# Kernel optimization log

Measured on AMD Instinct MI355X. Metric: run time of the kernel, lower is better.

## Reference

```python
import jax, jax.numpy as jnp
import numpy as np

H, W = 16, 16  # input_resolution
NUM_HEADS = 16
DIM = 512


def build_relative_position_index(h, w):
    coords = np.stack(np.meshgrid(np.arange(h), np.arange(w), indexing='ij'))  # [2,h,w]
    cf = coords.reshape(2, -1)
    rel = cf[:, :, None] - cf[:, None, :]            # [2,N,N]
    rel = rel.transpose(1, 2, 0).astype(np.int32)    # [N,N,2]
    rel[:, :, 0] += h - 1
    rel[:, :, 1] += w - 1
    rel[:, :, 0] *= 2 * w - 1
    return jnp.asarray(rel.sum(-1).reshape(-1), dtype=jnp.int32)  # [N*N]


def setup_inputs() -> dict:
    key = jax.random.key(0)
    ks = jax.random.split(key, 6)
    B, N, C = 128, H * W, DIM
    x = jax.random.normal(ks[0], (B, N, C), dtype=jnp.float32)
    qkv_w = jax.random.normal(ks[1], (3 * C, C), dtype=jnp.float32) * (C ** -0.5)
    qkv_b = jax.random.normal(ks[2], (3 * C,), dtype=jnp.float32) * 0.02
    proj_w = jax.random.normal(ks[3], (C, C), dtype=jnp.float32) * (C ** -0.5)
    proj_b = jax.random.normal(ks[4], (C,), dtype=jnp.float32) * 0.02
    bias_table = jax.random.normal(ks[5], ((2 * H - 1) * (2 * W - 1), NUM_HEADS), dtype=jnp.float32) * 0.02
    rel_index = build_relative_position_index(H, W)
    return {"x": x, "qkv_w": qkv_w, "qkv_b": qkv_b, "proj_w": proj_w,
            "proj_b": proj_b, "bias_table": bias_table, "rel_index": rel_index}


def reference(x, qkv_w, qkv_b, proj_w, proj_b, bias_table, rel_index):
    B, N, C = x.shape
    h = NUM_HEADS
    hd = C // h
    scale = hd ** -0.5
    # qkv projection: [B,N,3C] -> [3,B,h,N,hd]
    qkv = (jnp.einsum('bnc,oc->bno', x, qkv_w) + qkv_b)
    qkv = qkv.reshape(B, N, 3, h, hd).transpose(2, 0, 3, 1, 4)
    q, k, v = qkv[0], qkv[1], qkv[2]
    # relative position bias: gather [N*N,h] -> [1,h,N,N]
    bias = bias_table[rel_index].reshape(N, N, h).transpose(2, 0, 1)[None]
    attn = jnp.einsum('bhnd,bhmd->bhnm', q * scale, k) + bias
    attn = jax.nn.softmax(attn, axis=-1)
    out = jnp.einsum('bhnm,bhmd->bhnd', attn, v)     # [B,h,N,hd]
    out = out.transpose(0, 2, 1, 3).reshape(B, N, C)
    return jnp.einsum('bnc,oc->bno', out, proj_w) + proj_b
```

## Files before the change

### kernel.cpp

```cpp
#include <hip/hip_runtime.h>

typedef __bf16 bf16_t;
typedef __bf16 bf16x8 __attribute__((ext_vector_type(8)));
typedef float f32x4 __attribute__((ext_vector_type(4)));

#define MFMA_16x16x32(a, b, c) __builtin_amdgcn_mfma_f32_16x16x32_bf16((a), (b), (c), 0, 0, 0)

__device__ inline bf16x8 cvt8(const float* __restrict__ p) {
  bf16x8 r;
#pragma unroll
  for (int j = 0; j < 8; j++) r[j] = (bf16_t)p[j];
  return r;
}

__device__ inline void load_lds16(const bf16_t* g, bf16_t* l) {
  __builtin_amdgcn_global_load_lds(
      (const __attribute__((address_space(1))) void*)g,
      (__attribute__((address_space(3))) void*)l, 16, 0, 0);
}

__global__ __launch_bounds__(256) void convert_k(
    const float* __restrict__ x, const float* __restrict__ qkv_w,
    const float* __restrict__ proj_w,
    bf16_t* __restrict__ xbf, bf16_t* __restrict__ wqkvbf,
    bf16_t* __restrict__ wprojbf) {
  size_t base = ((size_t)blockIdx.x * 256 + threadIdx.x) * 8;
  if (base < 16777216) {
    *(bf16x8*)(xbf + base) = cvt8(x + base);
  } else if (base < 17563648) {
    size_t o = base - 16777216;
    *(bf16x8*)(wqkvbf + o) = cvt8(qkv_w + o);
  } else {
    size_t o = base - 17563648;
    *(bf16x8*)(wprojbf + o) = cvt8(proj_w + o);
  }
}

__global__ __launch_bounds__(256) void bias_gather_k(
    const float* __restrict__ table, const int* __restrict__ rel,
    float* __restrict__ biasws) {
  int idx = blockIdx.x * 256 + threadIdx.x;
  int h = idx >> 16;
  int rem = idx & 65535;
  int qb = rem >> 12;
  int ct = (rem >> 8) & 15;
  int L = (rem >> 2) & 63;
  int r = idx & 3;
  int q = qb * 16 + (L & 15);
  int k = ct * 16 + (L >> 4) * 4 + r;
  biasws[idx] = table[rel[q * 256 + k] * 16 + h];
}

#define PH_OPEN() __builtin_amdgcn_s_setprio(1)

#define PH_CLOSE()                                        \
  do {                                                    \
    __builtin_amdgcn_s_setprio(0);                        \
    asm volatile("s_waitcnt lgkmcnt(0)" ::: "memory");    \
    __builtin_amdgcn_sched_barrier(0);                    \
    __builtin_amdgcn_s_barrier();                         \
    __builtin_amdgcn_sched_barrier(0);                    \
  } while (0)

#define GATE4()                                           \
  do {                                                    \
    __builtin_amdgcn_s_setprio(0);                        \
    asm volatile("s_waitcnt vmcnt(4)" ::: "memory");      \
    __builtin_amdgcn_s_barrier();                         \
    __builtin_amdgcn_sched_barrier(0);                    \
  } while (0)

#define GATE0()                                           \
  do {                                                    \
    __builtin_amdgcn_s_setprio(0);                        \
    asm volatile("s_waitcnt vmcnt(0)" ::: "memory");      \
    __builtin_amdgcn_s_barrier();                         \
    __builtin_amdgcn_sched_barrier(0);                    \
  } while (0)

#define STG2(src, dst, c)                                                        \
  do {                                                                           \
    load_lds16((src) + (c)*32768, (dst) + (c)*4096);                             \
    load_lds16((src) + ((c) + 1) * 32768, (dst) + ((c) + 1) * 4096);             \
  } while (0)

#define RDA(dst, buf, ibase)                                                     \
  _Pragma("unroll") for (int i = 0; i < 4; ++i) {                                \
    dst[i][0] = *(const bf16x8*)&As[(buf)*16384 + a0 + ((ibase) + i) * 1024];    \
    dst[i][1] = *(const bf16x8*)&As[(buf)*16384 + a1 + ((ibase) + i) * 1024];    \
  }
#define RDB(dst, buf, jbase)                                                     \
  _Pragma("unroll") for (int j = 0; j < 2; ++j) {                                \
    dst[j][0] = *(const bf16x8*)&Bs[(buf)*16384 + b0 + ((jbase) + j) * 1024];    \
    dst[j][1] = *(const bf16x8*)&Bs[(buf)*16384 + b1 + ((jbase) + j) * 1024];    \
  }

#define MFQ(Af, Bf, I0, J0)                                                      \
  _Pragma("unroll") for (int i = 0; i < 4; ++i) _Pragma("unroll")                \
      for (int j = 0; j < 2; ++j) {                                              \
    acc[(I0) + i][(J0) + j] =                                                    \
        MFMA_16x16x32(Af[i][0], Bf[j][0], acc[(I0) + i][(J0) + j]);              \
    acc[(I0) + i][(J0) + j] =                                                    \
        MFMA_16x16x32(Af[i][1], Bf[j][1], acc[(I0) + i][(J0) + j]);              \
  }

#define GEMM_SETUP(Ap, Wp)                                                       \
  __shared__ bf16_t As[2 * 16384];                                               \
  __shared__ bf16_t Bs[2 * 16384];                                               \
  const int t = threadIdx.x;                                                     \
  const int w = t >> 6, L = t & 63;                                              \
  const int wm = w >> 2, wn = w & 3;                                             \
  const int lrow = L & 15, lq = L >> 4;                                          \
  const int srow = t >> 3;                                                       \
  const int sslot = (t & 7) ^ (srow & 7);                                        \
  const bf16_t* ga = (Ap) + (size_t)(m0 + srow) * 512 + sslot * 8;               \
  const bf16_t* gb = (Wp) + (size_t)(n0 + srow) * 512 + sslot * 8;               \
  bf16_t* la = As + t * 8;                                                       \
  bf16_t* lb = Bs + t * 8;                                                       \
  const int m8 = (lrow & 7) * 8;                                                 \
  const int a0 = (wm * 128 + lrow) * 64 + ((lq * 8) ^ m8);                       \
  const int a1 = (wm * 128 + lrow) * 64 + ((32 + lq * 8) ^ m8);                  \
  const int b0 = (wn * 64 + lrow) * 64 + ((lq * 8) ^ m8);                        \
  const int b1 = (wn * 64 + lrow) * 64 + ((32 + lq * 8) ^ m8);

#define PROLOGUE()                                                               \
  STG2(ga, la, 0); STG2(ga, la, 2);                                              \
  STG2(gb, lb, 0); STG2(gb, lb, 2);                                              \
  STG2(ga + 64, la + 16384, 0); STG2(ga + 64, la + 16384, 2);                    \
  asm volatile("s_waitcnt vmcnt(4)" ::: "memory");                               \
  __builtin_amdgcn_s_barrier();                                                  \
  __builtin_amdgcn_sched_barrier(0);

#define HALF_STEADY(CUR, LBDST, LADST, GBP, GAP)                                 \
  {                                                                              \
    bf16x8 fal[4][2], fbl[2][2], fah[4][2], fbh[2][2];                           \
    RDA(fal, CUR, 0); RDB(fbl, CUR, 0); RDB(fbh, CUR, 2);                        \
    STG2(GBP, LBDST, 0);                                                         \
    PH_OPEN(); MFQ(fal, fbl, 0, 0); PH_CLOSE();                                  \
    RDA(fah, CUR, 4);                                                            \
    STG2(GBP, LBDST, 2);                                                         \
    PH_OPEN(); MFQ(fal, fbh, 0, 2); PH_CLOSE();                                  \
    STG2(GAP, LADST, 0);                                                         \
    PH_OPEN(); MFQ(fah, fbh, 4, 2); PH_CLOSE();                                  \
    STG2(GAP, LADST, 2);                                                         \
    PH_OPEN(); MFQ(fah, fbl, 4, 0); GATE4();                                     \
  }

#define GEMM_LOOP()                                                              \
  {                                                                              \
    const bf16_t* gA = ga + 128;                                       \
    const bf16_t* gB = gb + 64;                                        \
    _Pragma("unroll 1") for (int G = 0; G < 3; ++G) {                            \
      HALF_STEADY(0, lb + 16384, la, gB, gA)                                     \
      HALF_STEADY(1, lb, la + 16384, gB + 64, gA + 64)                           \
      gA += 128; gB += 128;                                                      \
    }                                                                            \
    {            \
      bf16x8 fal[4][2], fbl[2][2], fah[4][2], fbh[2][2];                         \
      RDA(fal, 0, 0); RDB(fbl, 0, 0); RDB(fbh, 0, 2);                            \
      STG2(gB, lb + 16384, 0);                                                   \
      PH_OPEN(); MFQ(fal, fbl, 0, 0); PH_CLOSE();                                \
      RDA(fah, 0, 4);                                                            \
      STG2(gB, lb + 16384, 2);                                                   \
      PH_OPEN(); MFQ(fal, fbh, 0, 2); PH_CLOSE();                                \
      PH_OPEN(); MFQ(fah, fbh, 4, 2); PH_CLOSE();                                \
      PH_OPEN(); MFQ(fah, fbl, 4, 0); GATE0();                                   \
    }                                                                            \
    {                               \
      bf16x8 fal[4][2], fbl[2][2], fah[4][2], fbh[2][2];                         \
      RDA(fal, 1, 0); RDB(fbl, 1, 0); RDB(fbh, 1, 2);                            \
      PH_OPEN(); MFQ(fal, fbl, 0, 0); PH_CLOSE();                                \
      RDA(fah, 1, 4);                                                            \
      PH_OPEN(); MFQ(fal, fbh, 0, 2); PH_CLOSE();                                \
      PH_OPEN(); MFQ(fah, fbh, 4, 2); PH_CLOSE();                                \
      PH_OPEN(); MFQ(fah, fbl, 4, 0);                                            \
      __builtin_amdgcn_s_setprio(0);                                             \
      __builtin_amdgcn_sched_barrier(0);                                         \
    }                                                                            \
  }

__global__ __launch_bounds__(512, 2) void qkv_gemm256_k(
    const bf16_t* __restrict__ A, const bf16_t* __restrict__ W,
    const float* __restrict__ Bvec,
    bf16_t* __restrict__ qws, bf16_t* __restrict__ kws, bf16_t* __restrict__ vws) {
  const int id = blockIdx.x;
  const int wg = (id & 7) * 96 + (id >> 3);
  const int mt = wg / 6, nt = wg % 6;
  const int m0 = mt * 256, n0 = nt * 256;

  GEMM_SETUP(A, W);

  f32x4 acc[8][4];
#pragma unroll
  for (int jj = 0; jj < 4; ++jj) {
    float bv = Bvec[n0 + wn * 64 + jj * 16 + lrow];
#pragma unroll
    for (int i = 0; i < 8; ++i) acc[i][jj] = (f32x4){bv, bv, bv, bv};
  }

  PROLOGUE();
  GEMM_LOOP();

  const int col0 = n0 + wn * 64;
  const int s = col0 >> 9;
  bf16_t* dst = (s == 0) ? qws : (s == 1) ? kws : vws;
  const float mul = (s == 0) ? 0.17677669529663687f : 1.0f;
#pragma unroll
  for (int jj = 0; jj < 4; ++jj) {
    int o = col0 + jj * 16 + lrow;
    int rem = o & 511;
    int hh = rem >> 5, d = rem & 31;
#pragma unroll
    for (int i = 0; i < 8; ++i) {
#pragma unroll
      for (int r = 0; r < 4; ++r) {
        int m = m0 + wm * 128 + i * 16 + lq * 4 + r;
        int b = m >> 8, n = m & 255;
        dst[(size_t)(((b * 16 + hh) * 256 + n) << 5) + d] =
            (bf16_t)(acc[i][jj][r] * mul);
      }
    }
  }
}

__global__ __launch_bounds__(512, 2) void proj_gemm256_k(
    const bf16_t* __restrict__ A, const bf16_t* __restrict__ W,
    const float* __restrict__ Bvec, float* __restrict__ out) {
  const int id = blockIdx.x;
  const int lin = (id & 7) * 32 + (id >> 3);
  const int mt = lin >> 1, nt = lin & 1;
  const int m0 = mt * 256, n0 = nt * 256;

  GEMM_SETUP(A, W);

  f32x4 acc[8][4];
#pragma unroll
  for (int jj = 0; jj < 4; ++jj) {
    float bv = Bvec[n0 + wn * 64 + jj * 16 + lrow];
#pragma unroll
    for (int i = 0; i < 8; ++i) acc[i][jj] = (f32x4){bv, bv, bv, bv};
  }

  PROLOGUE();
  GEMM_LOOP();

#pragma unroll
  for (int jj = 0; jj < 4; ++jj) {
    int o = n0 + wn * 64 + jj * 16 + lrow;
#pragma unroll
    for (int i = 0; i < 8; ++i) {
#pragma unroll
      for (int r = 0; r < 4; ++r) {
        int m = m0 + wm * 128 + i * 16 + lq * 4 + r;
        out[(size_t)m * 512 + o] = acc[i][jj][r];
      }
    }
  }
}

__global__ __launch_bounds__(256) void attn_k(
    const bf16_t* __restrict__ qws, const bf16_t* __restrict__ kws,
    const bf16_t* __restrict__ vws, const float* __restrict__ biasws,
    bf16_t* __restrict__ aows) {
  __shared__ __align__(16) bf16_t Vs[32 * 264];

  const int bh = blockIdx.x;
  const int h = bh & 15, b = bh >> 4;

  const int t = threadIdx.x;
  const int w = t >> 6, L = t & 63;
  const int lrow = L & 15, lq = L >> 4;

  const bf16_t* kbase = kws + (size_t)bh * 8192;
  const bf16_t* vbase = vws + (size_t)bh * 8192;

#pragma unroll
  for (int c = 0; c < 4; c++) {
    bf16x8 vv = *(const bf16x8*)(vbase + t * 32 + c * 8);
#pragma unroll
    for (int j = 0; j < 8; j++) Vs[(c * 8 + j) * 264 + t] = vv[j];
  }
  __syncthreads();

  const int idxA = ((2 * (lq & 1)) * 16 + lrow) * 4;
  const int idxB = idxA + 64;
  const bool gsel = (lq < 2);

  const float* bbw = biasws + h * 65536 + (w * 4) * 4096;

#pragma unroll 1
  for (int s = 0; s < 4; ++s) {
    const int qrow0 = w * 64 + s * 16;
    const bf16_t* qbase = qws + (size_t)bh * 8192 + qrow0 * 32;
    bf16x8 qf = *(const bf16x8*)(qbase + lrow * 32 + lq * 8);
    const float* bb = bbw + s * 4096;

    f32x4 S[16];
#pragma unroll
    for (int ct = 0; ct < 16; ct++) {
      bf16x8 kf = *(const bf16x8*)(kbase + (ct * 16 + lrow) * 32 + lq * 8);
      f32x4 bi = *(const f32x4*)(bb + ct * 256 + L * 4);
      S[ct] = MFMA_16x16x32(kf, qf, bi);
    }

    float sm = 0.f;
#pragma unroll
    for (int ct = 0; ct < 16; ct++)
#pragma unroll
      for (int r = 0; r < 4; r++) {
        float e = __expf(S[ct][r]);
        S[ct][r] = e;
        sm += e;
      }
    sm += __shfl_xor(sm, 16, 64);
    sm += __shfl_xor(sm, 32, 64);
    const float inv = 1.0f / sm;

    int pd[16][2];
#pragma unroll
    for (int ct = 0; ct < 16; ct++) {
#pragma unroll
      for (int j = 0; j < 2; j++) {
        float lo = S[ct][2 * j] * inv;
        float hi = S[ct][2 * j + 1] * inv;
        int d;
        asm("v_cvt_pk_bf16_f32 %0, %1, %2" : "=v"(d) : "v"(lo), "v"(hi));
        pd[ct][j] = d;
      }
    }

    f32x4 O0 = {}, O1 = {};
#pragma unroll
    for (int kt = 0; kt < 8; kt++) {
      int rA0 = __builtin_amdgcn_ds_bpermute(idxA, pd[2 * kt][0]);
      int rA1 = __builtin_amdgcn_ds_bpermute(idxA, pd[2 * kt][1]);
      int rA2 = __builtin_amdgcn_ds_bpermute(idxB, pd[2 * kt][0]);
      int rA3 = __builtin_amdgcn_ds_bpermute(idxB, pd[2 * kt][1]);
      int rB0 = __builtin_amdgcn_ds_bpermute(idxA, pd[2 * kt + 1][0]);
      int rB1 = __builtin_amdgcn_ds_bpermute(idxA, pd[2 * kt + 1][1]);
      int rB2 = __builtin_amdgcn_ds_bpermute(idxB, pd[2 * kt + 1][0]);
      int rB3 = __builtin_amdgcn_ds_bpermute(idxB, pd[2 * kt + 1][1]);
      int4 Di;
      Di.x = gsel ? rA0 : rB0;
      Di.y = gsel ? rA1 : rB1;
      Di.z = gsel ? rA2 : rB2;
      Di.w = gsel ? rA3 : rB3;
      bf16x8 pf = *reinterpret_cast<bf16x8*>(&Di);
      bf16x8 v0 = *(const bf16x8*)&Vs[lrow * 264 + kt * 32 + lq * 8];
      bf16x8 v1 = *(const bf16x8*)&Vs[(16 + lrow) * 264 + kt * 32 + lq * 8];
      O0 = MFMA_16x16x32(pf, v0, O0);
      O1 = MFMA_16x16x32(pf, v1, O1);
    }

    bf16_t* obase = aows + (size_t)(b * 256 + qrow0) * 512 + h * 32;
#pragma unroll
    for (int r = 0; r < 4; r++) {
      int rl = lq * 4 + r;
      obase[rl * 512 + lrow] = (bf16_t)(O0[r]);
      obase[rl * 512 + 16 + lrow] = (bf16_t)(O1[r]);
    }
  }
}

extern "C" void kernel_launch(void* const* d_in, const int* in_sizes, int n_in,
                              void* d_out, int out_size, void* d_ws, size_t ws_size,
                              hipStream_t stream) {
  (void)in_sizes; (void)n_in; (void)out_size; (void)ws_size;
  const float* x      = (const float*)d_in[0];
  const float* qkv_w  = (const float*)d_in[1];
  const float* qkv_b  = (const float*)d_in[2];
  const float* proj_w = (const float*)d_in[3];
  const float* proj_b = (const float*)d_in[4];
  const float* table  = (const float*)d_in[5];
  const int*   rel    = (const int*)d_in[6];

  const size_t QKV_ELEMS = 16777216;
  bf16_t* qws     = (bf16_t*)d_ws;
  bf16_t* kws     = qws + QKV_ELEMS;
  bf16_t* vws     = kws + QKV_ELEMS;
  float*  biasws  = (float*)(vws + QKV_ELEMS);
  bf16_t* wqkvbf  = (bf16_t*)(biasws + 1048576);
  bf16_t* wprojbf = wqkvbf + 786432;
  bf16_t* xbf     = wprojbf + 262144;
  bf16_t* aows    = xbf;
  float*  out     = (float*)d_out;

  convert_k<<<8704, 256, 0, stream>>>(x, qkv_w, proj_w, xbf, wqkvbf, wprojbf);
  bias_gather_k<<<4096, 256, 0, stream>>>(table, rel, biasws);
  qkv_gemm256_k<<<768, 512, 0, stream>>>(xbf, wqkvbf, qkv_b, qws, kws, vws);
  attn_k<<<2048, 256, 0, stream>>>(qws, kws, vws, biasws, aows);
  proj_gemm256_k<<<256, 512, 0, stream>>>(aows, wprojbf, proj_b, out);
}
```

Measured before the change: 295.8 us.

## Shrink GEMM tiles to 128x128, fuse prep kernels, use exp2 softmax with deferred normalization

Both GEMMs move from 256x256 tiles with 512 threads to 128x128 tiles with 256 threads, giving more blocks for better CU fill and shorter tails at the cost of less data reuse per tile. The conversion and bias-gather kernels are merged into one launch to save a launch. Softmax now uses raw v_exp_f32 (base 2), with log2e folded into the q scale and the bias table. Normalization moves from every probability to the final output rows via a bpermute of the inverse sum, and the row sum uses vector partial sums.

```diff
diff --git a/kernel.cpp b/kernel.cpp
--- a/kernel.cpp
+++ b/kernel.cpp
@@ -5,6 +5,7 @@
 typedef float f32x4 __attribute__((ext_vector_type(4)));
 
 #define MFMA_16x16x32(a, b, c) __builtin_amdgcn_mfma_f32_16x16x32_bf16((a), (b), (c), 0, 0, 0)
+#define LOG2E 1.4426950408889634f
 
 __device__ inline bf16x8 cvt8(const float* __restrict__ p) {
   bf16x8 r;
@@ -19,36 +20,36 @@
       (__attribute__((address_space(3))) void*)l, 16, 0, 0);
 }
 
-__global__ __launch_bounds__(256) void convert_k(
+__global__ __launch_bounds__(256) void prep_k(
     const float* __restrict__ x, const float* __restrict__ qkv_w,
-    const float* __restrict__ proj_w,
+    const float* __restrict__ proj_w, const float* __restrict__ table,
+    const int* __restrict__ rel,
     bf16_t* __restrict__ xbf, bf16_t* __restrict__ wqkvbf,
-    bf16_t* __restrict__ wprojbf) {
-  size_t base = ((size_t)blockIdx.x * 256 + threadIdx.x) * 8;
-  if (base < 16777216) {
-    *(bf16x8*)(xbf + base) = cvt8(x + base);
-  } else if (base < 17563648) {
-    size_t o = base - 16777216;
-    *(bf16x8*)(wqkvbf + o) = cvt8(qkv_w + o);
+    bf16_t* __restrict__ wprojbf, float* __restrict__ biasws) {
+  const int bid = blockIdx.x;
+  if (bid < 8704) {
+    size_t base = ((size_t)bid * 256 + threadIdx.x) * 8;
+    if (base < 16777216) {
+      *(bf16x8*)(xbf + base) = cvt8(x + base);
+    } else if (base < 17563648) {
+      size_t o = base - 16777216;
+      *(bf16x8*)(wqkvbf + o) = cvt8(qkv_w + o);
+    } else {
+      size_t o = base - 17563648;
+      *(bf16x8*)(wprojbf + o) = cvt8(proj_w + o);
+    }
   } else {
-    size_t o = base - 17563648;
-    *(bf16x8*)(wprojbf + o) = cvt8(proj_w + o);
-  }
-}
-
-__global__ __launch_bounds__(256) void bias_gather_k(
-    const float* __restrict__ table, const int* __restrict__ rel,
-    float* __restrict__ biasws) {
-  int idx = blockIdx.x * 256 + threadIdx.x;
-  int h = idx >> 16;
-  int rem = idx & 65535;
-  int qb = rem >> 12;
-  int ct = (rem >> 8) & 15;
-  int L = (rem >> 2) & 63;
-  int r = idx & 3;
-  int q = qb * 16 + (L & 15);
-  int k = ct * 16 + (L >> 4) * 4 + r;
-  biasws[idx] = table[rel[q * 256 + k] * 16 + h];
+    int idx = (bid - 8704) * 256 + threadIdx.x;
+    int h = idx >> 16;
+    int rem = idx & 65535;
+    int qb = rem >> 12;
+    int ct = (rem >> 8) & 15;
+    int L = (rem >> 2) & 63;
+    int r = idx & 3;
+    int q = qb * 16 + (L & 15);
+    int k = ct * 16 + (L >> 4) * 4 + r;
+    biasws[idx] = table[rel[q * 256 + k] * 16 + h] * LOG2E;
+  }
 }
 
 #define PH_OPEN() __builtin_amdgcn_s_setprio(1)
@@ -80,23 +81,23 @@
 
 #define STG2(src, dst, c)                                                        \
   do {                                                                           \
-    load_lds16((src) + (c)*32768, (dst) + (c)*4096);                             \
-    load_lds16((src) + ((c) + 1) * 32768, (dst) + ((c) + 1) * 4096);             \
+    load_lds16((src) + (c)*16384, (dst) + (c)*2048);                             \
+    load_lds16((src) + ((c) + 1) * 16384, (dst) + ((c) + 1) * 2048);             \
   } while (0)
 
-#define RDA(dst, buf, ibase)                                                     \
-  _Pragma("unroll") for (int i = 0; i < 4; ++i) {                                \
-    dst[i][0] = *(const bf16x8*)&As[(buf)*16384 + a0 + ((ibase) + i) * 1024];    \
-    dst[i][1] = *(const bf16x8*)&As[(buf)*16384 + a1 + ((ibase) + i) * 1024];    \
-  }
-#define RDB(dst, buf, jbase)                                                     \
+#define RDA2(dst, buf, ibase)                                                    \
+  _Pragma("unroll") for (int i = 0; i < 2; ++i) {                                \
+    dst[i][0] = *(const bf16x8*)&As[(buf)*8192 + a0 + ((ibase) + i) * 1024];     \
+    dst[i][1] = *(const bf16x8*)&As[(buf)*8192 + a1 + ((ibase) + i) * 1024];     \
+  }
+#define RDB2(dst, buf, jbase)                                                    \
   _Pragma("unroll") for (int j = 0; j < 2; ++j) {                                \
-    dst[j][0] = *(const bf16x8*)&Bs[(buf)*16384 + b0 + ((jbase) + j) * 1024];    \
-    dst[j][1] = *(const bf16x8*)&Bs[(buf)*16384 + b1 + ((jbase) + j) * 1024];    \
-  }
-
-#define MFQ(Af, Bf, I0, J0)                                                      \
-  _Pragma("unroll") for (int i = 0; i < 4; ++i) _Pragma("unroll")                \
+    dst[j][0] = *(const bf16x8*)&Bs[(buf)*8192 + b0 + ((jbase) + j) * 1024];     \
+    dst[j][1] = *(const bf16x8*)&Bs[(buf)*8192 + b1 + ((jbase) + j) * 1024];     \
+  }
+
+#define MFQ2(Af, Bf, I0, J0)                                                     \
+  _Pragma("unroll") for (int i = 0; i < 2; ++i) _Pragma("unroll")                \
       for (int j = 0; j < 2; ++j) {                                              \
     acc[(I0) + i][(J0) + j] =                                                    \
         MFMA_16x16x32(Af[i][0], Bf[j][0], acc[(I0) + i][(J0) + j]);              \
@@ -105,11 +106,11 @@
   }
 
 #define GEMM_SETUP(Ap, Wp)                                                       \
-  __shared__ bf16_t As[2 * 16384];                                               \
-  __shared__ bf16_t Bs[2 * 16384];                                               \
+  __shared__ bf16_t As[2 * 8192];                                                \
+  __shared__ bf16_t Bs[2 * 8192];                                                \
   const int t = threadIdx.x;                                                     \
   const int w = t >> 6, L = t & 63;                                              \
-  const int wm = w >> 2, wn = w & 3;                                             \
+  const int wm = w >> 1, wn = w & 1;                                             \
   const int lrow = L & 15, lq = L >> 4;                                          \
   const int srow = t >> 3;                                                       \
   const int sslot = (t & 7) ^ (srow & 7);                                        \
@@ -118,32 +119,32 @@
   bf16_t* la = As + t * 8;                                                       \
   bf16_t* lb = Bs + t * 8;                                                       \
   const int m8 = (lrow & 7) * 8;                                                 \
-  const int a0 = (wm * 128 + lrow) * 64 + ((lq * 8) ^ m8);                       \
-  const int a1 = (wm * 128 + lrow) * 64 + ((32 + lq * 8) ^ m8);                  \
+  const int a0 = (wm * 64 + lrow) * 64 + ((lq * 8) ^ m8);                        \
+  const int a1 = (wm * 64 + lrow) * 64 + ((32 + lq * 8) ^ m8);                   \
   const int b0 = (wn * 64 + lrow) * 64 + ((lq * 8) ^ m8);                        \
   const int b1 = (wn * 64 + lrow) * 64 + ((32 + lq * 8) ^ m8);
 
 #define PROLOGUE()                                                               \
   STG2(ga, la, 0); STG2(ga, la, 2);                                              \
   STG2(gb, lb, 0); STG2(gb, lb, 2);                                              \
-  STG2(ga + 64, la + 16384, 0); STG2(ga + 64, la + 16384, 2);                    \
+  STG2(ga + 64, la + 8192, 0); STG2(ga + 64, la + 8192, 2);                      \
   asm volatile("s_waitcnt vmcnt(4)" ::: "memory");                               \
   __builtin_amdgcn_s_barrier();                                                  \
   __builtin_amdgcn_sched_barrier(0);
 
 #define HALF_STEADY(CUR, LBDST, LADST, GBP, GAP)                                 \
   {                                                                              \
-    bf16x8 fal[4][2], fbl[2][2], fah[4][2], fbh[2][2];                           \
-    RDA(fal, CUR, 0); RDB(fbl, CUR, 0); RDB(fbh, CUR, 2);                        \
+    bf16x8 fal[2][2], fbl[2][2], fah[2][2], fbh[2][2];                           \
+    RDA2(fal, CUR, 0); RDB2(fbl, CUR, 0); RDB2(fbh, CUR, 2);                     \
     STG2(GBP, LBDST, 0);                                                         \
-    PH_OPEN(); MFQ(fal, fbl, 0, 0); PH_CLOSE();                                  \
-    RDA(fah, CUR, 4);                                                            \
+    PH_OPEN(); MFQ2(fal, fbl, 0, 0); PH_CLOSE();                                 \
+    RDA2(fah, CUR, 2);                                                           \
     STG2(GBP, LBDST, 2);                                                         \
-    PH_OPEN(); MFQ(fal, fbh, 0, 2); PH_CLOSE();                                  \
+    PH_OPEN(); MFQ2(fal, fbh, 0, 2); PH_CLOSE();                                 \
     STG2(GAP, LADST, 0);                                                         \
-    PH_OPEN(); MFQ(fah, fbh, 4, 2); PH_CLOSE();                                  \
+    PH_OPEN(); MFQ2(fah, fbh, 2, 2); PH_CLOSE();                                 \
     STG2(GAP, LADST, 2);                                                         \
-    PH_OPEN(); MFQ(fah, fbl, 4, 0); GATE4();                                     \
+    PH_OPEN(); MFQ2(fah, fbl, 2, 0); GATE4();                                    \
   }
 
 #define GEMM_LOOP()                                                              \
@@ -151,51 +152,51 @@
     const bf16_t* gA = ga + 128;                                       \
     const bf16_t* gB = gb + 64;                                        \
     _Pragma("unroll 1") for (int G = 0; G < 3; ++G) {                            \
-      HALF_STEADY(0, lb + 16384, la, gB, gA)                                     \
-      HALF_STEADY(1, lb, la + 16384, gB + 64, gA + 64)                           \
+      HALF_STEADY(0, lb + 8192, la, gB, gA)                                      \
+      HALF_STEADY(1, lb, la + 8192, gB + 64, gA + 64)                            \
       gA += 128; gB += 128;                                                      \
     }                                                                            \
     {            \
-      bf16x8 fal[4][2], fbl[2][2], fah[4][2], fbh[2][2];                         \
-      RDA(fal, 0, 0); RDB(fbl, 0, 0); RDB(fbh, 0, 2);                            \
-      STG2(gB, lb + 16384, 0);                                                   \
-      PH_OPEN(); MFQ(fal, fbl, 0, 0); PH_CLOSE();                                \
-      RDA(fah, 0, 4);                                                            \
-      STG2(gB, lb + 16384, 2);                                                   \
-      PH_OPEN(); MFQ(fal, fbh, 0, 2); PH_CLOSE();                                \
-      PH_OPEN(); MFQ(fah, fbh, 4, 2); PH_CLOSE();                                \
-      PH_OPEN(); MFQ(fah, fbl, 4, 0); GATE0();                                   \
+      bf16x8 fal[2][2], fbl[2][2], fah[2][2], fbh[2][2];                         \
+      RDA2(fal, 0, 0); RDB2(fbl, 0, 0); RDB2(fbh, 0, 2);                         \
+      STG2(gB, lb + 8192, 0);                                                    \
+      PH_OPEN(); MFQ2(fal, fbl, 0, 0); PH_CLOSE();                               \
+      RDA2(fah, 0, 2);                                                           \
+      STG2(gB, lb + 8192, 2);                                                    \
+      PH_OPEN(); MFQ2(fal, fbh, 0, 2); PH_CLOSE();                               \
+      PH_OPEN(); MFQ2(fah, fbh, 2, 2); PH_CLOSE();                               \
+      PH_OPEN(); MFQ2(fah, fbl, 2, 0); GATE0();                                  \
     }                                                                            \
     {                               \
-      bf16x8 fal[4][2], fbl[2][2], fah[4][2], fbh[2][2];                         \
-      RDA(fal, 1, 0); RDB(fbl, 1, 0); RDB(fbh, 1, 2);                            \
-      PH_OPEN(); MFQ(fal, fbl, 0, 0); PH_CLOSE();                                \
-      RDA(fah, 1, 4);                                                            \
-      PH_OPEN(); MFQ(fal, fbh, 0, 2); PH_CLOSE();                                \
-      PH_OPEN(); MFQ(fah, fbh, 4, 2); PH_CLOSE();                                \
-      PH_OPEN(); MFQ(fah, fbl, 4, 0);                                            \
+      bf16x8 fal[2][2], fbl[2][2], fah[2][2], fbh[2][2];                         \
+      RDA2(fal, 1, 0); RDB2(fbl, 1, 0); RDB2(fbh, 1, 2);                         \
+      PH_OPEN(); MFQ2(fal, fbl, 0, 0); PH_CLOSE();                               \
+      RDA2(fah, 1, 2);                                                           \
+      PH_OPEN(); MFQ2(fal, fbh, 0, 2); PH_CLOSE();                               \
+      PH_OPEN(); MFQ2(fah, fbh, 2, 2); PH_CLOSE();                               \
+      PH_OPEN(); MFQ2(fah, fbl, 2, 0);                                           \
       __builtin_amdgcn_s_setprio(0);                                             \
       __builtin_amdgcn_sched_barrier(0);                                         \
     }                                                                            \
   }
 
-__global__ __launch_bounds__(512, 2) void qkv_gemm256_k(
+__global__ __launch_bounds__(256, 2) void qkv_gemm128_k(
     const bf16_t* __restrict__ A, const bf16_t* __restrict__ W,
     const float* __restrict__ Bvec,
     bf16_t* __restrict__ qws, bf16_t* __restrict__ kws, bf16_t* __restrict__ vws) {
   const int id = blockIdx.x;
-  const int wg = (id & 7) * 96 + (id >> 3);
-  const int mt = wg / 6, nt = wg % 6;
-  const int m0 = mt * 256, n0 = nt * 256;
+  const int wg = (id & 7) * 384 + (id >> 3);
+  const int mt = wg / 12, nt = wg % 12;
+  const int m0 = mt * 128, n0 = nt * 128;
 
   GEMM_SETUP(A, W);
 
-  f32x4 acc[8][4];
+  f32x4 acc[4][4];
 #pragma unroll
   for (int jj = 0; jj < 4; ++jj) {
     float bv = Bvec[n0 + wn * 64 + jj * 16 + lrow];
 #pragma unroll
-    for (int i = 0; i < 8; ++i) acc[i][jj] = (f32x4){bv, bv, bv, bv};
+    for (int i = 0; i < 4; ++i) acc[i][jj] = (f32x4){bv, bv, bv, bv};
   }
 
   PROLOGUE();
@@ -204,17 +205,17 @@
   const int col0 = n0 + wn * 64;
   const int s = col0 >> 9;
   bf16_t* dst = (s == 0) ? qws : (s == 1) ? kws : vws;
-  const float mul = (s == 0) ? 0.17677669529663687f : 1.0f;
+  const float mul = (s == 0) ? 0.17677669529663687f * LOG2E : 1.0f;
 #pragma unroll
   for (int jj = 0; jj < 4; ++jj) {
     int o = col0 + jj * 16 + lrow;
     int rem = o & 511;
     int hh = rem >> 5, d = rem & 31;
 #pragma unroll
-    for (int i = 0; i < 8; ++i) {
+    for (int i = 0; i < 4; ++i) {
 #pragma unroll
       for (int r = 0; r < 4; ++r) {
-        int m = m0 + wm * 128 + i * 16 + lq * 4 + r;
+        int m = m0 + wm * 64 + i * 16 + lq * 4 + r;
         int b = m >> 8, n = m & 255;
         dst[(size_t)(((b * 16 + hh) * 256 + n) << 5) + d] =
             (bf16_t)(acc[i][jj][r] * mul);
@@ -223,22 +224,22 @@
   }
 }
 
-__global__ __launch_bounds__(512, 2) void proj_gemm256_k(
+__global__ __launch_bounds__(256, 2) void proj_gemm128_k(
     const bf16_t* __restrict__ A, const bf16_t* __restrict__ W,
     const float* __restrict__ Bvec, float* __restrict__ out) {
   const int id = blockIdx.x;
-  const int lin = (id & 7) * 32 + (id >> 3);
-  const int mt = lin >> 1, nt = lin & 1;
-  const int m0 = mt * 256, n0 = nt * 256;
+  const int wg = (id & 7) * 128 + (id >> 3);
+  const int mt = wg >> 2, nt = wg & 3;
+  const int m0 = mt * 128, n0 = nt * 128;
 
   GEMM_SETUP(A, W);
 
-  f32x4 acc[8][4];
+  f32x4 acc[4][4];
 #pragma unroll
   for (int jj = 0; jj < 4; ++jj) {
     float bv = Bvec[n0 + wn * 64 + jj * 16 + lrow];
 #pragma unroll
-    for (int i = 0; i < 8; ++i) acc[i][jj] = (f32x4){bv, bv, bv, bv};
+    for (int i = 0; i < 4; ++i) acc[i][jj] = (f32x4){bv, bv, bv, bv};
   }
 
   PROLOGUE();
@@ -248,10 +249,10 @@
   for (int jj = 0; jj < 4; ++jj) {
     int o = n0 + wn * 64 + jj * 16 + lrow;
 #pragma unroll
-    for (int i = 0; i < 8; ++i) {
+    for (int i = 0; i < 4; ++i) {
 #pragma unroll
       for (int r = 0; r < 4; ++r) {
-        int m = m0 + wm * 128 + i * 16 + lq * 4 + r;
+        int m = m0 + wm * 64 + i * 16 + lq * 4 + r;
         out[(size_t)m * 512 + o] = acc[i][jj][r];
       }
     }
@@ -303,15 +304,18 @@
       S[ct] = MFMA_16x16x32(kf, qf, bi);
     }
 
-    float sm = 0.f;
-#pragma unroll
-    for (int ct = 0; ct < 16; ct++)
+    f32x4 sv = {};
+#pragma unroll
+    for (int ct = 0; ct < 16; ct++) {
 #pragma unroll
       for (int r = 0; r < 4; r++) {
-        float e = __expf(S[ct][r]);
+        float e;
+        asm("v_exp_f32 %0, %1" : "=v"(e) : "v"(S[ct][r]));
         S[ct][r] = e;
-        sm += e;
       }
+      sv += S[ct];
+    }
+    float sm = (sv[0] + sv[1]) + (sv[2] + sv[3]);
     sm += __shfl_xor(sm, 16, 64);
     sm += __shfl_xor(sm, 32, 64);
     const float inv = 1.0f / sm;
@@ -321,10 +325,9 @@
     for (int ct = 0; ct < 16; ct++) {
 #pragma unroll
       for (int j = 0; j < 2; j++) {
-        float lo = S[ct][2 * j] * inv;
-        float hi = S[ct][2 * j + 1] * inv;
         int d;
-        asm("v_cvt_pk_bf16_f32 %0, %1, %2" : "=v"(d) : "v"(lo), "v"(hi));
+        asm("v_cvt_pk_bf16_f32 %0, %1, %2"
+            : "=v"(d) : "v"(S[ct][2 * j]), "v"(S[ct][2 * j + 1]));
         pd[ct][j] = d;
       }
     }
@@ -355,9 +358,11 @@
     bf16_t* obase = aows + (size_t)(b * 256 + qrow0) * 512 + h * 32;
 #pragma unroll
     for (int r = 0; r < 4; r++) {
+      float invO = __int_as_float(
+          __builtin_amdgcn_ds_bpermute((lq * 4 + r) * 4, __float_as_int(inv)));
       int rl = lq * 4 + r;
-      obase[rl * 512 + lrow] = (bf16_t)(O0[r]);
-      obase[rl * 512 + 16 + lrow] = (bf16_t)(O1[r]);
+      obase[rl * 512 + lrow] = (bf16_t)(O0[r] * invO);
+      obase[rl * 512 + 16 + lrow] = (bf16_t)(O1[r] * invO);
     }
   }
 }
@@ -385,9 +390,9 @@
   bf16_t* aows    = xbf;
   float*  out     = (float*)d_out;
 
-  convert_k<<<8704, 256, 0, stream>>>(x, qkv_w, proj_w, xbf, wqkvbf, wprojbf);
-  bias_gather_k<<<4096, 256, 0, stream>>>(table, rel, biasws);
-  qkv_gemm256_k<<<768, 512, 0, stream>>>(xbf, wqkvbf, qkv_b, qws, kws, vws);
+  prep_k<<<12800, 256, 0, stream>>>(x, qkv_w, proj_w, table, rel,
+                                    xbf, wqkvbf, wprojbf, biasws);
+  qkv_gemm128_k<<<3072, 256, 0, stream>>>(xbf, wqkvbf, qkv_b, qws, kws, vws);
   attn_k<<<2048, 256, 0, stream>>>(qws, kws, vws, biasws, aows);
-  proj_gemm256_k<<<256, 512, 0, stream>>>(aows, wprojbf, proj_b, out);
-}
+  proj_gemm128_k<<<1024, 256, 0, stream>>>(aows, wprojbf, proj_b, out);
+}
```

After: 323.0 us. +9.2%, slower.
